# Performance work log

Hardware: AMD Instinct MI355X
Metric: run time of the kernel (lower is better)

Reference implementation:

```python
import jax, jax.numpy as jnp
import numpy as np


def setup_inputs() -> dict:
    key = jax.random.key(0)
    k1, k2 = jax.random.split(key)
    B, N, D = 4, 2048, 1024
    context = jax.random.normal(k1, (B, N, D), dtype=jnp.float32)
    # Dense(embedding_dim*3): kernel [D, 3D], bias [3D] (glorot-ish scale)
    W_qkv = jax.random.normal(k2, (D, 3 * D), dtype=jnp.float32) * (1.0 / np.sqrt(D))
    b_qkv = jnp.zeros((3 * D,), dtype=jnp.float32)
    return {"context": context, "W_qkv": W_qkv, "b_qkv": b_qkv}


def reference(context, W_qkv, b_qkv):
    B, N, D = context.shape
    qkv = context @ W_qkv + b_qkv                       # [B, N, 3D]
    q, k, v = jnp.split(qkv, 3, axis=-1)                # each [B, N, D]
    scores = jnp.einsum("bnd,bmd->bnm", q, k)           # [B, N, N]
    # Faithful quirk: original divides by sqrt(scores.shape[-1]) == sqrt(N)
    scores = scores / jnp.asarray(np.sqrt(N), dtype=scores.dtype)
    causal = jnp.tril(jnp.ones((N, N), dtype=jnp.float32))  # lower-triangular
    scores = jnp.where(causal == 0, -jnp.inf, scores)
    probs = jax.nn.softmax(scores, axis=-1)             # [B, N, N]
    out = jnp.einsum("bnm,bmd->bnd", probs, v)          # [B, N, D]
    return out
```

## Files before the change

### kernel.cpp

```cpp
#include <hip/hip_runtime.h>
#include <cstdint>
#include <cstddef>


typedef __attribute__((ext_vector_type(8))) __bf16 bf16x8;
typedef __attribute__((ext_vector_type(4))) float f32x4;

__device__ inline unsigned short f2bf(float f) {
  unsigned u = __float_as_uint(f);
  u = (u + 0x7FFFu + ((u >> 16) & 1u)) >> 16;
  return (unsigned short)u;
}

__device__ inline void gld16(const void* g, void* l) {
  __builtin_amdgcn_global_load_lds(
      (const __attribute__((address_space(1))) unsigned int*)g,
      (__attribute__((address_space(3))) unsigned int*)l, 16, 0, 0);
}


__device__ inline void stage_Ahalf(const unsigned short* Agb, int k0,
                                   unsigned short* Abuf, int half,
                                   int wave, int lrow, int lcol) {
#pragma unroll
  for (int i = 0; i < 2; i++) {
    const int c = wave * 2 + i;
    const int rg = ((c >> 3) << 7) + ((c & 7) << 3) + (half << 6);
    gld16(Agb + (size_t)(rg + lrow) * 1024 + k0 + lcol, Abuf + rg * 64);
  }
}

__device__ inline void stage_Bhalf(const unsigned short* Bgb, int k0,
                                   unsigned short* Bbuf, int half,
                                   int wave, int lrow, int lcol) {
#pragma unroll
  for (int i = 0; i < 2; i++) {
    const int c = wave * 2 + i;
    const int rg = ((c >> 2) << 6) + ((c & 3) << 3) + (half << 5);
    gld16(Bgb + (size_t)(rg + lrow) * 1024 + k0 + lcol, Bbuf + rg * 64);
  }
}

__device__ inline void read_Ahalf(const unsigned short* buf, int wm, int half,
                                  int lane, bf16x8 (&a)[4][2]) {
#pragma unroll
  for (int ks = 0; ks < 2; ks++) {
    const int csw = ((((ks << 2) + (lane >> 4)) ^ (lane & 7)) << 3);
#pragma unroll
    for (int mi = 0; mi < 4; mi++) {
      const int R = wm * 128 + half * 64 + mi * 16 + (lane & 15);
      a[mi][ks] = *(const bf16x8*)&buf[R * 64 + csw];
    }
  }
}

__device__ inline void read_Bhalf(const unsigned short* buf, int wn, int half,
                                  int lane, bf16x8 (&b)[2][2]) {
#pragma unroll
  for (int ks = 0; ks < 2; ks++) {
    const int csw = ((((ks << 2) + (lane >> 4)) ^ (lane & 7)) << 3);
#pragma unroll
    for (int nj = 0; nj < 2; nj++) {
      const int R = wn * 64 + half * 32 + nj * 16 + (lane & 15);
      b[nj][ks] = *(const bf16x8*)&buf[R * 64 + csw];
    }
  }
}

__device__ inline void mma_quad(const bf16x8 (&a)[4][2], const bf16x8 (&b)[2][2],
                                f32x4 (&acc)[8][4], const int ah, const int bh) {
#pragma unroll
  for (int ks = 0; ks < 2; ks++)
#pragma unroll
    for (int mi = 0; mi < 4; mi++)
#pragma unroll
      for (int nj = 0; nj < 2; nj++)
        acc[ah * 4 + mi][bh * 2 + nj] = __builtin_amdgcn_mfma_f32_16x16x32_bf16(
            b[nj][ks], a[mi][ks], acc[ah * 4 + mi][bh * 2 + nj], 0, 0, 0);
}

#define QKV_FENCE()                         \
  __builtin_amdgcn_s_barrier();             \
  asm volatile("" ::: "memory");            \
  __builtin_amdgcn_sched_barrier(0)

template <bool STAGE, int V0, int V1, int V2>
__device__ inline void qkv_tile(const unsigned short* Agb, const unsigned short* Bgb,
                                int k0n, const unsigned short* Ar, const unsigned short* Br,
                                unsigned short* Aw, unsigned short* Bw,
                                int wave, int lane, int wm, int wn,
                                f32x4 (&acc)[8][4]) {
  const int lrow = lane >> 3;
  const int lcol = ((lane & 7) ^ lrow) * 8;
  bf16x8 aLo[4][2], aHi[4][2], bLo[2][2], bHi[2][2];
  if (STAGE) stage_Ahalf(Agb, k0n, Aw, 0, wave, lrow, lcol);
  asm volatile("s_waitcnt vmcnt(%0)" ::"i"(V0) : "memory");
  QKV_FENCE();
  read_Ahalf(Ar, wm, 0, lane, aLo);
  read_Bhalf(Br, wn, 0, lane, bLo);
  __builtin_amdgcn_s_setprio(1);
  mma_quad(aLo, bLo, acc, 0, 0);
  __builtin_amdgcn_s_setprio(0);
  __builtin_amdgcn_sched_barrier(0);
  __builtin_amdgcn_s_barrier();
  if (STAGE) stage_Bhalf(Bgb, k0n, Bw, 0, wave, lrow, lcol);
  asm volatile("s_waitcnt vmcnt(%0)" ::"i"(V1) : "memory");
  QKV_FENCE();
  read_Bhalf(Br, wn, 1, lane, bHi);
  __builtin_amdgcn_s_setprio(1);
  mma_quad(aLo, bHi, acc, 0, 1);
  __builtin_amdgcn_s_setprio(0);
  __builtin_amdgcn_sched_barrier(0);
  __builtin_amdgcn_s_barrier();
  if (STAGE) stage_Bhalf(Bgb, k0n, Bw, 1, wave, lrow, lcol);
  asm volatile("s_waitcnt vmcnt(%0)" ::"i"(V2) : "memory");
  QKV_FENCE();
  read_Ahalf(Ar, wm, 1, lane, aHi);
  __builtin_amdgcn_s_setprio(1);
  mma_quad(aHi, bHi, acc, 1, 1);
  __builtin_amdgcn_s_setprio(0);
  __builtin_amdgcn_sched_barrier(0);
  __builtin_amdgcn_s_barrier();
  if (STAGE) stage_Ahalf(Agb, k0n, Aw, 1, wave, lrow, lcol);
  __builtin_amdgcn_s_setprio(1);
  mma_quad(aHi, bLo, acc, 1, 0);
  __builtin_amdgcn_s_setprio(0);
  __builtin_amdgcn_sched_barrier(0);
  __builtin_amdgcn_s_barrier();
}

__global__ __launch_bounds__(512, 2) void k_gemm_qkv(
    const unsigned short* __restrict__ A, const unsigned short* __restrict__ Wt,
    const float* __restrict__ bias, unsigned short* __restrict__ qk,
    unsigned short* __restrict__ vT) {
  __shared__ unsigned short sA[2 * 16384];
  __shared__ unsigned short sB[2 * 16384];
  const int bid = blockIdx.y * 12 + blockIdx.x;
  const int swz = (bid & 7) * 48 + (bid >> 3);
  const int nb = swz % 12, mb = swz / 12;
  const int tN0 = nb * 256, tM0 = mb * 256;
  const unsigned short* Agb = A + (size_t)tM0 * 1024;
  const unsigned short* Bgb = Wt + (size_t)tN0 * 1024;
  const int lane = threadIdx.x & 63, wave = threadIdx.x >> 6;
  const int wm = wave >> 2, wn = wave & 3;
  const int lrow = lane >> 3, lcol = ((lane & 7) ^ lrow) * 8;

  f32x4 acc[8][4];
#pragma unroll
  for (int mi = 0; mi < 8; mi++)
#pragma unroll
    for (int nj = 0; nj < 4; nj++) acc[mi][nj] = (f32x4)(0.f);

  stage_Ahalf(Agb, 0, sA, 0, wave, lrow, lcol);
  stage_Bhalf(Bgb, 0, sB, 0, wave, lrow, lcol);
  stage_Bhalf(Bgb, 0, sB, 1, wave, lrow, lcol);
  stage_Ahalf(Agb, 0, sA, 1, wave, lrow, lcol);

  for (int kt = 0; kt < 15; kt++) {
    const unsigned short* Ar = sA + (kt & 1) * 16384;
    const unsigned short* Br = sB + (kt & 1) * 16384;
    unsigned short* Aw = sA + ((kt + 1) & 1) * 16384;
    unsigned short* Bw = sB + ((kt + 1) & 1) * 16384;
    qkv_tile<true, 6, 6, 6>(Agb, Bgb, (kt + 1) * 64, Ar, Br, Aw, Bw,
                            wave, lane, wm, wn, acc);
  }
  qkv_tile<false, 4, 2, 0>(Agb, Bgb, 0, sA + 16384, sB + 16384, sA, sB,
                           wave, lane, wm, wn, acc);

  const int l16 = lane & 15, rq = lane >> 4;
  int m0 = tM0 + wm * 128;
  asm volatile("" : "+v"(m0));
  if (tN0 < 2048) {
#pragma unroll
    for (int mi = 0; mi < 8; mi++) {
      const int m = m0 + mi * 16 + l16;
#pragma unroll
      for (int nj = 0; nj < 4; nj++) {
        const int n = tN0 + wn * 64 + nj * 16 + rq * 4;
        const float4 bv = *(const float4*)&bias[n];
        ushort4 o;
        o.x = f2bf(acc[mi][nj][0] + bv.x);
        o.y = f2bf(acc[mi][nj][1] + bv.y);
        o.z = f2bf(acc[mi][nj][2] + bv.z);
        o.w = f2bf(acc[mi][nj][3] + bv.w);
        *(ushort4*)&qk[(size_t)m * 2048 + n] = o;
      }
    }
  } else {
    const int d0b = tN0 - 2048 + wn * 64;
#pragma unroll
    for (int mi = 0; mi < 8; mi++) {
      const int m = m0 + mi * 16 + l16;
      const int b = m >> 11, ns = m & 2047;
#pragma unroll
      for (int nj = 0; nj < 4; nj++) {
        const int d0 = d0b + nj * 16 + rq * 4;
        const float4 bv = *(const float4*)&bias[2048 + d0];
#pragma unroll
        for (int r = 0; r < 4; r++)
          vT[((size_t)(b * 1024 + d0 + r)) * 2048 + ns] =
              f2bf(acc[mi][nj][r] + ((const float*)&bv)[r]);
      }
    }
  }
}

__device__ inline void compute_tiles64(const unsigned short* As, const unsigned short* Bs,
                                       int lane, int ry, int rx, f32x4 acc[4][2]) {
#pragma unroll
  for (int kk = 0; kk < 64; kk += 32) {
    const int cbase = (kk >> 3) + (lane >> 4);
    const int csw = ((cbase ^ (lane & 7)) << 3);
    bf16x8 a[4], b[2];
#pragma unroll
    for (int mi = 0; mi < 4; mi++)
      a[mi] = *(const bf16x8*)&As[(ry + mi * 16 + (lane & 15)) * 64 + csw];
#pragma unroll
    for (int nj = 0; nj < 2; nj++)
      b[nj] = *(const bf16x8*)&Bs[(rx + nj * 16 + (lane & 15)) * 64 + csw];
#pragma unroll
    for (int mi = 0; mi < 4; mi++)
#pragma unroll
      for (int nj = 0; nj < 2; nj++)
        acc[mi][nj] = __builtin_amdgcn_mfma_f32_16x16x32_bf16(b[nj], a[mi], acc[mi][nj], 0, 0, 0);
  }
}

__device__ inline void mma_mainloop64(unsigned short* As, unsigned short* Bs,
                                      const unsigned short* Abase, long strideA,
                                      const unsigned short* Bbase, long strideB,
                                      int kIters, f32x4 acc[4][2]) {
  const int lane = threadIdx.x & 63, wave = threadIdx.x >> 6;
  const int ry = (wave >> 1) * 64, rx = (wave & 1) * 32;
  const int lrow = lane >> 3;
  const int lcol = ((lane & 7) ^ lrow) * 8;
#pragma unroll
  for (int mi = 0; mi < 4; mi++)
#pragma unroll
    for (int nj = 0; nj < 2; nj++) acc[mi][nj] = (f32x4)(0.f);
  for (int kt = 0; kt < kIters; kt++) {
    const int k0 = kt * 64;
    __syncthreads();
#pragma unroll
    for (int c = 0; c < 4; c++) {
      const int q = wave * 4 + c;
      const int row = q * 8 + lrow;
      gld16(Abase + (size_t)row * strideA + k0 + lcol, &As[q * 512]);
    }
#pragma unroll
    for (int c = 0; c < 2; c++) {
      const int q = wave * 2 + c;
      const int row = q * 8 + lrow;
      gld16(Bbase + (size_t)row * strideB + k0 + lcol, &Bs[q * 512]);
    }
    __syncthreads();
    compute_tiles64(As, Bs, lane, ry, rx, acc);
  }
}


__global__ void k_convert(const float* __restrict__ x, unsigned short* __restrict__ y, int n4) {
  int i = blockIdx.x * blockDim.x + threadIdx.x;
  if (i >= n4) return;
  float4 v = ((const float4*)x)[i];
  ushort4 o;
  o.x = f2bf(v.x); o.y = f2bf(v.y); o.z = f2bf(v.z); o.w = f2bf(v.w);
  ((ushort4*)y)[i] = o;
}

__global__ void k_transpose_w(const float* __restrict__ W, unsigned short* __restrict__ Wt) {
  __shared__ unsigned short sm[64 * 65];
  const int n0 = blockIdx.x * 64;
  const int k0 = blockIdx.y * 64;
  for (int i = threadIdx.x; i < 4096; i += 256) {
    int r = i >> 6, c = i & 63;
    sm[c * 65 + r] = f2bf(W[(size_t)(k0 + r) * 3072 + n0 + c]);
  }
  __syncthreads();
  for (int i = threadIdx.x; i < 4096; i += 256) {
    int r = i >> 6, c = i & 63;
    Wt[(size_t)(n0 + r) * 1024 + k0 + c] = sm[r * 65 + c];
  }
}


__global__ __launch_bounds__(256) void k_scores(const unsigned short* __restrict__ qk,
                                                unsigned short* __restrict__ P,
                                                float* __restrict__ l, float scale) {
  __shared__ unsigned short As[128 * 64];
  __shared__ unsigned short Bs[64 * 64];
  const int t = blockIdx.x, b = blockIdx.z;
  int qb = (int)((sqrtf(4.0f * (float)t + 1.0f) - 1.0f) * 0.5f);
  while (qb * (qb + 1) > t) qb--;
  while ((qb + 1) * (qb + 2) <= t) qb++;
  const int kb2 = t - qb * (qb + 1);
  f32x4 acc[4][2];
  const unsigned short* Aq = qk + ((size_t)(b * 2048 + qb * 128)) * 2048;
  const unsigned short* Bk = qk + ((size_t)(b * 2048 + kb2 * 64)) * 2048 + 1024;
  mma_mainloop64(As, Bs, Aq, 2048, Bk, 2048, 16, acc);
  const int lane = threadIdx.x & 63, wave = threadIdx.x >> 6;
  const int ry = (wave >> 1) * 64, rx = (wave & 1) * 32;
  const int l16 = lane & 15, rq = lane >> 4;
  unsigned short* Pb = P + ((size_t)(b * 2048 + qb * 128)) * 2048 + (size_t)kb2 * 64;
  float* lb = l + b * 2048 + qb * 128;
#pragma unroll
  for (int mi = 0; mi < 4; mi++) {
    const int m_local = ry + mi * 16 + l16;
    const int qi = qb * 128 + m_local;
    float rowpart = 0.f;
#pragma unroll
    for (int nj = 0; nj < 2; nj++) {
      const int n_base = rx + nj * 16 + rq * 4;
      ushort4 o;
      float p;
#pragma unroll
      for (int r = 0; r < 4; r++) {
        const int kj = kb2 * 64 + n_base + r;
        p = (kj <= qi) ? __expf(acc[mi][nj][r] * scale) : 0.f;
        rowpart += p;
        ((unsigned short*)&o)[r] = f2bf(p);
      }
      *(ushort4*)&Pb[(size_t)m_local * 2048 + n_base] = o;
    }
    rowpart += __shfl_xor(rowpart, 16, 64);
    rowpart += __shfl_xor(rowpart, 32, 64);
    if (rq == 0) atomicAdd(&lb[m_local], rowpart);
  }
}

__global__ __launch_bounds__(256) void k_pv(const unsigned short* __restrict__ P,
                                            const unsigned short* __restrict__ vT,
                                            const float* __restrict__ l,
                                            float* __restrict__ out) {
  __shared__ unsigned short As[128 * 64];
  __shared__ unsigned short Bs[64 * 64];
  const int db2 = blockIdx.x, b = blockIdx.z;
  int qb = blockIdx.y;
  if (b & 2) qb = 15 - qb;
  f32x4 acc[4][2];
  const unsigned short* Ap = P + ((size_t)(b * 2048 + qb * 128)) * 2048;
  const unsigned short* Bv = vT + ((size_t)(b * 1024 + db2 * 64)) * 2048;
  mma_mainloop64(As, Bs, Ap, 2048, Bv, 2048, (qb + 1) * 2, acc);
  const int lane = threadIdx.x & 63, wave = threadIdx.x >> 6;
  const int ry = (wave >> 1) * 64, rx = (wave & 1) * 32;
  const int l16 = lane & 15, rq = lane >> 4;
  const float* lb = l + b * 2048 + qb * 128;
  float* ob = out + ((size_t)(b * 2048 + qb * 128)) * 1024 + db2 * 64;
#pragma unroll
  for (int mi = 0; mi < 4; mi++) {
    const int m_local = ry + mi * 16 + l16;
    const float inv = 1.0f / lb[m_local];
#pragma unroll
    for (int nj = 0; nj < 2; nj++) {
      const int n_base = rx + nj * 16 + rq * 4;
      float4 o;
      o.x = acc[mi][nj][0] * inv;
      o.y = acc[mi][nj][1] * inv;
      o.z = acc[mi][nj][2] * inv;
      o.w = acc[mi][nj][3] * inv;
      *(float4*)&ob[(size_t)m_local * 1024 + n_base] = o;
    }
  }
}


extern "C" void kernel_launch(void* const* d_in, const int* in_sizes, int n_in,
                              void* d_out, int out_size, void* d_ws, size_t ws_size,
                              hipStream_t stream) {
  const float* ctx  = (const float*)d_in[0];
  const float* W    = (const float*)d_in[1];
  const float* bias = (const float*)d_in[2];
  float* out = (float*)d_out;

  char* ws = (char*)d_ws;
  unsigned short* Actx = (unsigned short*)(ws + 0);
  unsigned short* Wt   = (unsigned short*)(ws + 16777216);
  unsigned short* qk   = (unsigned short*)(ws + 23068672);
  unsigned short* vT   = (unsigned short*)(ws + 56623104);
  unsigned short* P    = (unsigned short*)(ws + 73400320);
  float*          lsum = (float*)(ws + 106954752);

  hipMemsetAsync(lsum, 0, 4 * 2048 * sizeof(float), stream);
  k_convert<<<8192, 256, 0, stream>>>(ctx, Actx, (8192 * 1024) / 4);
  k_transpose_w<<<dim3(48, 16), 256, 0, stream>>>(W, Wt);
  k_gemm_qkv<<<dim3(12, 32), 512, 0, stream>>>(Actx, Wt, bias, qk, vT);
  k_scores<<<dim3(272, 1, 4), 256, 0, stream>>>(qk, P, lsum, 0.022097086912079608f);
  k_pv<<<dim3(16, 16, 4), 256, 0, stream>>>(P, vT, lsum, out);
}
```

Measured before the change: 251.2 us.

## Restructure QKV GEMM pipeline to stage half-tiles further ahead

Reorganizes the QKV projection GEMM main loop into a two-k-tile unrolled iteration. LDS fragment reads are issued before each MFMA phase, and global-to-LDS half-tile loads for tiles one and two steps ahead are interleaved between phases. The vmcnt waits move to only two points per iteration, so global loads get more time in flight. The cost is a more intricate buffer-reuse schedule that depends on exact waitcnt values and barrier placement for correctness.

```diff
diff --git a/kernel.cpp b/kernel.cpp
--- a/kernel.cpp
+++ b/kernel.cpp
@@ -79,54 +79,54 @@
             b[nj][ks], a[mi][ks], acc[ah * 4 + mi][bh * 2 + nj], 0, 0, 0);
 }
 
-#define QKV_FENCE()                         \
-  __builtin_amdgcn_s_barrier();             \
-  asm volatile("" ::: "memory");            \
-  __builtin_amdgcn_sched_barrier(0)
-
-template <bool STAGE, int V0, int V1, int V2>
-__device__ inline void qkv_tile(const unsigned short* Agb, const unsigned short* Bgb,
-                                int k0n, const unsigned short* Ar, const unsigned short* Br,
-                                unsigned short* Aw, unsigned short* Bw,
+#define QKV_MFMA_PHASE(AFRAG, BFRAG, AH, BH)        \
+  __builtin_amdgcn_s_barrier();                     \
+  asm volatile("s_waitcnt lgkmcnt(0)" ::: "memory"); \
+  __builtin_amdgcn_sched_barrier(0);                \
+  __builtin_amdgcn_s_setprio(1);                    \
+  mma_quad(AFRAG, BFRAG, acc, AH, BH);              \
+  __builtin_amdgcn_s_setprio(0);                    \
+  __builtin_amdgcn_sched_barrier(0);                \
+  __builtin_amdgcn_s_barrier()
+
+template <bool STG, int C4, int C8>
+__device__ inline void qkv_iter(const unsigned short* Agb, const unsigned short* Bgb,
+                                int k1, int k2, int k3,
+                                unsigned short* sA, unsigned short* sB,
                                 int wave, int lane, int wm, int wn,
                                 f32x4 (&acc)[8][4]) {
-  const int lrow = lane >> 3;
-  const int lcol = ((lane & 7) ^ lrow) * 8;
+  const int lrow = lane >> 3, lcol = ((lane & 7) ^ lrow) * 8;
+  unsigned short *A0 = sA, *A1 = sA + 16384, *B0 = sB, *B1 = sB + 16384;
   bf16x8 aLo[4][2], aHi[4][2], bLo[2][2], bHi[2][2];
-  if (STAGE) stage_Ahalf(Agb, k0n, Aw, 0, wave, lrow, lcol);
-  asm volatile("s_waitcnt vmcnt(%0)" ::"i"(V0) : "memory");
-  QKV_FENCE();
-  read_Ahalf(Ar, wm, 0, lane, aLo);
-  read_Bhalf(Br, wn, 0, lane, bLo);
-  __builtin_amdgcn_s_setprio(1);
-  mma_quad(aLo, bLo, acc, 0, 0);
-  __builtin_amdgcn_s_setprio(0);
-  __builtin_amdgcn_sched_barrier(0);
-  __builtin_amdgcn_s_barrier();
-  if (STAGE) stage_Bhalf(Bgb, k0n, Bw, 0, wave, lrow, lcol);
-  asm volatile("s_waitcnt vmcnt(%0)" ::"i"(V1) : "memory");
-  QKV_FENCE();
-  read_Bhalf(Br, wn, 1, lane, bHi);
-  __builtin_amdgcn_s_setprio(1);
-  mma_quad(aLo, bHi, acc, 0, 1);
-  __builtin_amdgcn_s_setprio(0);
-  __builtin_amdgcn_sched_barrier(0);
-  __builtin_amdgcn_s_barrier();
-  if (STAGE) stage_Bhalf(Bgb, k0n, Bw, 1, wave, lrow, lcol);
-  asm volatile("s_waitcnt vmcnt(%0)" ::"i"(V2) : "memory");
-  QKV_FENCE();
-  read_Ahalf(Ar, wm, 1, lane, aHi);
-  __builtin_amdgcn_s_setprio(1);
-  mma_quad(aHi, bHi, acc, 1, 1);
-  __builtin_amdgcn_s_setprio(0);
-  __builtin_amdgcn_sched_barrier(0);
-  __builtin_amdgcn_s_barrier();
-  if (STAGE) stage_Ahalf(Agb, k0n, Aw, 1, wave, lrow, lcol);
-  __builtin_amdgcn_s_setprio(1);
-  mma_quad(aHi, bLo, acc, 1, 0);
-  __builtin_amdgcn_s_setprio(0);
-  __builtin_amdgcn_sched_barrier(0);
-  __builtin_amdgcn_s_barrier();
+
+  read_Ahalf(A0, wm, 0, lane, aLo);
+  read_Bhalf(B0, wn, 0, lane, bLo);
+  stage_Ahalf(Agb, k1, A1, 1, wave, lrow, lcol);
+  QKV_MFMA_PHASE(aLo, bLo, 0, 0);
+  read_Bhalf(B0, wn, 1, lane, bHi);
+  if (STG) stage_Ahalf(Agb, k2, A0, 0, wave, lrow, lcol);
+  QKV_MFMA_PHASE(aLo, bHi, 0, 1);
+  read_Ahalf(A0, wm, 1, lane, aHi);
+  if (STG) stage_Bhalf(Bgb, k2, B0, 0, wave, lrow, lcol);
+  QKV_MFMA_PHASE(aHi, bHi, 1, 1);
+  if (STG) stage_Bhalf(Bgb, k2, B0, 1, wave, lrow, lcol);
+  if constexpr (C4 >= 0)
+    asm volatile("s_waitcnt vmcnt(%0)" ::"i"(C4) : "memory");
+  QKV_MFMA_PHASE(aHi, bLo, 1, 0);
+  read_Ahalf(A1, wm, 0, lane, aLo);
+  read_Bhalf(B1, wn, 0, lane, bLo);
+  if (STG) stage_Ahalf(Agb, k2, A0, 1, wave, lrow, lcol);
+  QKV_MFMA_PHASE(aLo, bLo, 0, 0);
+  read_Bhalf(B1, wn, 1, lane, bHi);
+  if (STG) stage_Ahalf(Agb, k3, A1, 0, wave, lrow, lcol);
+  QKV_MFMA_PHASE(aLo, bHi, 0, 1);
+  read_Ahalf(A1, wm, 1, lane, aHi);
+  if (STG) stage_Bhalf(Bgb, k3, B1, 0, wave, lrow, lcol);
+  QKV_MFMA_PHASE(aHi, bHi, 1, 1);
+  if (STG) stage_Bhalf(Bgb, k3, B1, 1, wave, lrow, lcol);
+  if constexpr (C8 >= 0)
+    asm volatile("s_waitcnt vmcnt(%0)" ::"i"(C8) : "memory");
+  QKV_MFMA_PHASE(aHi, bLo, 1, 0);
 }
 
 __global__ __launch_bounds__(512, 2) void k_gemm_qkv(
@@ -155,17 +155,16 @@
   stage_Bhalf(Bgb, 0, sB, 0, wave, lrow, lcol);
   stage_Bhalf(Bgb, 0, sB, 1, wave, lrow, lcol);
   stage_Ahalf(Agb, 0, sA, 1, wave, lrow, lcol);
-
-  for (int kt = 0; kt < 15; kt++) {
-    const unsigned short* Ar = sA + (kt & 1) * 16384;
-    const unsigned short* Br = sB + (kt & 1) * 16384;
-    unsigned short* Aw = sA + ((kt + 1) & 1) * 16384;
-    unsigned short* Bw = sB + ((kt + 1) & 1) * 16384;
-    qkv_tile<true, 6, 6, 6>(Agb, Bgb, (kt + 1) * 64, Ar, Br, Aw, Bw,
-                            wave, lane, wm, wn, acc);
-  }
-  qkv_tile<false, 4, 2, 0>(Agb, Bgb, 0, sA + 16384, sB + 16384, sA, sB,
-                           wave, lane, wm, wn, acc);
+  stage_Ahalf(Agb, 64, sA + 16384, 0, wave, lrow, lcol);
+  stage_Bhalf(Bgb, 64, sB + 16384, 0, wave, lrow, lcol);
+  stage_Bhalf(Bgb, 64, sB + 16384, 1, wave, lrow, lcol);
+  asm volatile("s_waitcnt vmcnt(6)" ::: "memory");
+  __builtin_amdgcn_s_barrier();
+
+  for (int i = 0; i < 7; i++)
+    qkv_iter<true, 6, 6>(Agb, Bgb, (2 * i + 1) * 64, (2 * i + 2) * 64,
+                         (2 * i + 3) * 64, sA, sB, wave, lane, wm, wn, acc);
+  qkv_iter<false, 0, -1>(Agb, Bgb, 15 * 64, 0, 0, sA, sB, wave, lane, wm, wn, acc);
 
   const int l16 = lane & 15, rq = lane >> 4;
   int m0 = tM0 + wm * 128;
```

After: 255.4 us. No clear change (+1.7%).
